# Optimization experiments

Measured on AMD Instinct MI355X. Metric: run time of the kernel, lower is better.

The kernel has to match this reference:

```python
import jax, jax.numpy as jnp
import numpy as np

B, LQ, LKV, D = 8, 2048, 2048, 1024

def setup_inputs() -> dict:
    key = jax.random.key(0)
    k1, k2, k3, k4, k5, k6, k7 = jax.random.split(key, 7)
    s = 1.0 / np.sqrt(D)
    return {
        "query": jax.random.normal(k1, (B, LQ, D), jnp.float32),
        "key": jax.random.normal(k2, (B, LKV, D), jnp.float32),
        "value": jax.random.normal(k3, (B, LKV, D), jnp.float32),
        "Wq": jax.random.uniform(k4, (D, D), jnp.float32, -s, s),
        "bq": jax.random.uniform(k5, (D,), jnp.float32, -s, s),
        "Wk": jax.random.uniform(k6, (D, D), jnp.float32, -s, s),
        "bk": jax.random.uniform(k7, (D,), jnp.float32, -s, s),
        "scale_factor": 32,
        "dropout_p": 0,
    }

def reference(query, key, value, Wq, bq, Wk, bk, scale_factor, dropout_p):
    # q/k linear projections (torch Linear: x @ W^T + b); v is used raw per the source
    q = jnp.einsum("bld,ed->ble", query, Wq) + bq
    k = jnp.einsum("bld,ed->ble", key, Wk) + bk
    scores = jnp.einsum("bqd,bkd->bqk", q, k) / jnp.float32(scale_factor)
    attn = jax.nn.softmax(scores, axis=-1)
    # dropout_p == 0 -> identity (deterministic baseline)
    return jnp.einsum("bqk,bkd->bqd", attn, value)
```

## Files before the change

### kernel.cpp

```cpp
#include <hip/hip_runtime.h>

typedef __bf16 bf16;
typedef __attribute__((ext_vector_type(4))) __bf16 bf16x4;
typedef __attribute__((ext_vector_type(8))) __bf16 bf16x8;
typedef __attribute__((ext_vector_type(4))) float f32x4;

__device__ __forceinline__ void gload_lds16(const void* g, void* l) {
  __builtin_amdgcn_global_load_lds(
      (const __attribute__((address_space(1))) unsigned int*)(unsigned long long)g,
      (__attribute__((address_space(3))) unsigned int*)(unsigned long long)l,
      16, 0, 0);
}

__global__ void cast_f32_bf16(const float* __restrict__ in, bf16* __restrict__ out, int n4) {
  int i = blockIdx.x * blockDim.x + threadIdx.x;
  if (i >= n4) return;
  float4 v = reinterpret_cast<const float4*>(in)[i];
  bf16x4 o;
  o[0] = (bf16)v.x; o[1] = (bf16)v.y; o[2] = (bf16)v.z; o[3] = (bf16)v.w;
  reinterpret_cast<bf16x4*>(out)[i] = o;
}

__global__ void transpose_cast(const float* __restrict__ V, bf16* __restrict__ VT,
                               int rows, int cols) {
  __shared__ bf16 tile[64][65];
  const int b = blockIdx.z;
  const float* Vb = V + (long)b * rows * cols;
  bf16* VTb = VT + (long)b * rows * cols;
  const int d0 = blockIdx.x * 64;
  const int k0 = blockIdx.y * 64;
  const int t = threadIdx.x;
  const int r = t >> 4;
  const int c4 = (t & 15) * 4;
#pragma unroll
  for (int p = 0; p < 4; ++p) {
    float4 v = *reinterpret_cast<const float4*>(&Vb[(long)(k0 + p * 16 + r) * cols + d0 + c4]);
    tile[p * 16 + r][c4 + 0] = (bf16)v.x;
    tile[p * 16 + r][c4 + 1] = (bf16)v.y;
    tile[p * 16 + r][c4 + 2] = (bf16)v.z;
    tile[p * 16 + r][c4 + 3] = (bf16)v.w;
  }
  __syncthreads();
#pragma unroll
  for (int p = 0; p < 4; ++p) {
    const int dd = p * 16 + r;
    bf16x4 o;
    o[0] = tile[c4 + 0][dd];
    o[1] = tile[c4 + 1][dd];
    o[2] = tile[c4 + 2][dd];
    o[3] = tile[c4 + 3][dd];
    *reinterpret_cast<bf16x4*>(&VTb[(long)(d0 + dd) * rows + k0 + c4]) = o;
  }
}

__global__ void softmax_rows(bf16* __restrict__ S) {
  const long row = blockIdx.x;
  bf16* p = S + row * 2048;
  const int t = threadIdx.x;
  const int wid = t >> 6;
  const int lane = t & 63;
  bf16x8 v = *reinterpret_cast<bf16x8*>(p + t * 8);
  float f[8];
  float m = -3.0e38f;
#pragma unroll
  for (int j = 0; j < 8; ++j) { f[j] = (float)v[j]; m = fmaxf(m, f[j]); }
#pragma unroll
  for (int off = 32; off >= 1; off >>= 1) m = fmaxf(m, __shfl_xor(m, off));
  __shared__ float redm[4], reds[4];
  if (lane == 0) redm[wid] = m;
  __syncthreads();
  m = fmaxf(fmaxf(redm[0], redm[1]), fmaxf(redm[2], redm[3]));
  float s = 0.f;
#pragma unroll
  for (int j = 0; j < 8; ++j) { f[j] = __expf(f[j] - m); s += f[j]; }
#pragma unroll
  for (int off = 32; off >= 1; off >>= 1) s += __shfl_xor(s, off);
  if (lane == 0) reds[wid] = s;
  __syncthreads();
  s = reds[0] + reds[1] + reds[2] + reds[3];
  const float inv = 1.0f / s;
  bf16x8 o;
#pragma unroll
  for (int j = 0; j < 8; ++j) o[j] = (bf16)(f[j] * inv);
  *reinterpret_cast<bf16x8*>(p + t * 8) = o;
}


#define BARRIER __builtin_amdgcn_s_barrier()
#define SCHED0 __builtin_amdgcn_sched_barrier(0)
#define VM4                                                \
  do {                                                     \
    asm volatile("s_waitcnt vmcnt(4)" ::: "memory");       \
  } while (0)

#define STAGE(buf, ko)                                     \
  {                                                        \
    bf16* l_ = ldsw + (buf) * 16384;                       \
    const long ko_ = (ko);                                 \
    gload_lds16(gA + ko_, l_);                             \
    gload_lds16(gA + ko_ + rK128, l_ + 4096);              \
    gload_lds16(gB + ko_, l_ + 8192);                      \
    gload_lds16(gB + ko_ + rK128, l_ + 12288);             \
  }

#define LOADA(dst, buf)                                                        \
  _Pragma("unroll") for (int m_ = 0; m_ < 8; ++m_)                             \
      dst[m_] = *reinterpret_cast<const bf16x8*>(aBase + (buf) * 16384 + m_ * 512);
#define LOADB(dst, buf)                                                        \
  _Pragma("unroll") for (int n_ = 0; n_ < 4; ++n_)                             \
      dst[n_] = *reinterpret_cast<const bf16x8*>(bBase + (buf) * 16384 + n_ * 512);

#define MFMA32(a_, b_)                                                         \
  _Pragma("unroll") for (int m_ = 0; m_ < 8; ++m_)                             \
  _Pragma("unroll") for (int n_ = 0; n_ < 4; ++n_)                             \
      acc[m_][n_] = __builtin_amdgcn_mfma_f32_16x16x32_bf16(                   \
          a_[m_], b_[n_], acc[m_][n_], 0, 0, 0);

#define ROT3 { int tmp_ = c0; c0 = c1; c1 = c2; c2 = tmp_; }

template <int MODE>
__global__ __launch_bounds__(512, 2)
void gemm_bt(const bf16* __restrict__ A, const bf16* __restrict__ Bm,
             const float* __restrict__ bias0, const float* __restrict__ bias1,
             void* __restrict__ Cvoid, const int* __restrict__ scale_ptr,
             int N, int K, long sA, long sB, long sC) {
  __shared__ bf16 lds[3][512][32];
  const int t = threadIdx.x;
  const int lane = t & 63;
  const int wid = t >> 6;
  const int wm = wid >> 2;
  const int wn = wid & 3;

  const int gx = gridDim.x, gy = gridDim.y;
  const int nwg = gx * gy * gridDim.z;
  int id = blockIdx.x + gx * (blockIdx.y + gy * blockIdx.z);
  {
    const int cpx = nwg >> 3;
    id = (id & 7) * cpx + (id >> 3);
  }
  const int bx = id % gx;
  const int by = (id / gx) % gy;
  const int bz = id / (gx * gy);

  const bf16* Ab = A + (long)bz * sA;
  const bf16* Bb = Bm + (long)bz * sB;
  const int tile_m = by * 256;
  const int tile_n = bx * 256;

  const int srow = t >> 2;
  const int soff = (((t & 3) ^ ((t >> 3) & 3)) << 3);
  const bf16* gA = Ab + (long)(tile_m + srow) * K + soff;
  const bf16* gB = Bb + (long)(tile_n + srow) * K + soff;
  const long rK128 = (long)K << 7;
  bf16* const ldsw = &lds[0][0][0] + wid * 512;

  const int frow = lane & 15;
  const int pko = (((lane >> 4) ^ ((lane >> 1) & 3)) << 3);
  const bf16* aBase = &lds[0][0][0] + (wm * 128 + frow) * 32 + pko;
  const bf16* bBase = &lds[0][0][0] + (256 + wn * 64 + frow) * 32 + pko;

  bf16x8 aX[8], bX[4], aY[8], bY[4];
  f32x4 acc[8][4] = {};

  const int NK = K >> 5;
  int c0 = 0, c1 = 1, c2 = 2;

  STAGE(0, 0)
  STAGE(1, 32)
  VM4;
  BARRIER;
  SCHED0;
  LOADA(aX, 0)
  LOADB(bX, 0)

  for (int kt = 0; kt < NK; kt += 2) {
    {
      const long tt = (kt + 2 < NK) ? (long)(kt + 2) : (long)(NK - 1);
      STAGE(c2, tt << 5)
    }
    VM4;
    BARRIER;
    SCHED0;
    LOADA(aY, c1)
    LOADB(bY, c1)
    MFMA32(aX, bX)
    ROT3
    {
      const long tt = (kt + 3 < NK) ? (long)(kt + 3) : (long)(NK - 1);
      STAGE(c2, tt << 5)
    }
    VM4;
    BARRIER;
    SCHED0;
    LOADA(aX, c1)
    LOADB(bX, c1)
    MFMA32(aY, bY)
    ROT3
  }

  float scl = 1.0f;
  if (MODE == 1) {
    const int iv = scale_ptr[0];
    const float fv = __int_as_float(iv);
    const float sv = (iv > 0 && iv < (1 << 20)) ? (float)iv : fv;
    scl = 1.0f / sv;
  }
  const int rb = tile_m + wm * 128 + ((lane >> 4) << 2);
  const int cb = tile_n + wn * 64 + (lane & 15);
  if (MODE == 2) {
    float* C = reinterpret_cast<float*>(Cvoid) + (long)bz * sC;
#pragma unroll
    for (int mf = 0; mf < 8; ++mf)
#pragma unroll
      for (int nf = 0; nf < 4; ++nf)
#pragma unroll
        for (int r = 0; r < 4; ++r)
          C[(long)(rb + mf * 16 + r) * N + (cb + nf * 16)] = acc[mf][nf][r];
  } else {
    bf16* C = reinterpret_cast<bf16*>(Cvoid) + (long)bz * sC;
    const float* bias = (MODE == 0) ? (bz ? bias1 : bias0) : nullptr;
#pragma unroll
    for (int nf = 0; nf < 4; ++nf) {
      const int col = cb + nf * 16;
      const float bv = (MODE == 0) ? bias[col] : 0.0f;
#pragma unroll
      for (int mf = 0; mf < 8; ++mf)
#pragma unroll
        for (int r = 0; r < 4; ++r)
          C[(long)(rb + mf * 16 + r) * N + col] = (bf16)(acc[mf][nf][r] * scl + bv);
    }
  }
}

extern "C" void kernel_launch(void* const* d_in, const int* in_sizes, int n_in,
                              void* d_out, int out_size, void* d_ws, size_t ws_size,
                              hipStream_t stream) {
  (void)in_sizes; (void)n_in; (void)out_size; (void)ws_size;
  const float* query = (const float*)d_in[0];
  const float* key   = (const float*)d_in[1];
  const float* value = (const float*)d_in[2];
  const float* Wq    = (const float*)d_in[3];
  const float* bq    = (const float*)d_in[4];
  const float* Wk    = (const float*)d_in[5];
  const float* bk    = (const float*)d_in[6];
  const int*   scale = (const int*)d_in[7];

  const int L = 2048, D = 1024;
  char* ws = (char*)d_ws;
  bf16* q_cast = (bf16*)ws;
  bf16* k_cast = q_cast + (long)16384 * 1024;
  bf16* S      = q_cast;
  bf16* Qp     = (bf16*)(ws + (size_t)67108864);
  bf16* Kp     = (bf16*)(ws + (size_t)100663296);
  bf16* VT     = (bf16*)(ws + (size_t)134217728);
  bf16* Wqb    = (bf16*)(ws + (size_t)167772160);
  bf16* Wkb    = (bf16*)(ws + (size_t)169869312);

  cast_f32_bf16<<<16384, 256, 0, stream>>>(query, q_cast, 4194304);
  cast_f32_bf16<<<16384, 256, 0, stream>>>(key,   k_cast, 4194304);
  cast_f32_bf16<<<1024,  256, 0, stream>>>(Wq, Wqb, 262144);
  cast_f32_bf16<<<1024,  256, 0, stream>>>(Wk, Wkb, 262144);
  transpose_cast<<<dim3(16, 32, 8), 256, 0, stream>>>(value, VT, 2048, 1024);

  gemm_bt<0><<<dim3(4, 64, 2), 512, 0, stream>>>(q_cast, Wqb, bq, bk, Qp, nullptr,
                                                 1024, 1024,
                                                 16777216L, 1048576L, 16777216L);
  gemm_bt<1><<<dim3(8, 8, 8), 512, 0, stream>>>(Qp, Kp, nullptr, nullptr, S, scale,
                                                2048, 1024,
                                                (long)L * D, (long)L * D, (long)L * L);
  softmax_rows<<<16384, 256, 0, stream>>>(S);
  gemm_bt<2><<<dim3(4, 8, 8), 512, 0, stream>>>(S, VT, nullptr, nullptr, d_out, nullptr,
                                                1024, 2048,
                                                (long)L * L, (long)D * L, (long)L * D);
}
```

Baseline: 299.9 us.

## Switch GEMM to 32x32x16 MFMA with 64-wide K double-buffered pipeline

Replaces the 16x16x32 MFMA tiles with 32x32x16 MFMA, so each wave holds 4x2 accumulators of 16 floats and reads fewer LDS fragments per FLOP. The K loop now stages 64-wide K chunks as two 32-wide halves into a double buffer, where the old code used a triple buffer of 32-wide chunks. It also adds explicit lgkmcnt waits and s_setprio around the MFMA blocks. The aim is to cut LDS read traffic and improve MFMA issue density, at the cost of extra barriers per iteration and a more serialized load-then-compute schedule.

```diff
diff --git a/kernel.cpp b/kernel.cpp
--- a/kernel.cpp
+++ b/kernel.cpp
@@ -3,7 +3,7 @@
 typedef __bf16 bf16;
 typedef __attribute__((ext_vector_type(4))) __bf16 bf16x4;
 typedef __attribute__((ext_vector_type(8))) __bf16 bf16x8;
-typedef __attribute__((ext_vector_type(4))) float f32x4;
+typedef __attribute__((ext_vector_type(16))) float f32x16;
 
 __device__ __forceinline__ void gload_lds16(const void* g, void* l) {
   __builtin_amdgcn_global_load_lds(
@@ -87,36 +87,53 @@
 
 
 #define BARRIER __builtin_amdgcn_s_barrier()
-#define SCHED0 __builtin_amdgcn_sched_barrier(0)
+#define LGKM0                                              \
+  do {                                                     \
+    asm volatile("s_waitcnt lgkmcnt(0)" ::: "memory");     \
+    __builtin_amdgcn_sched_barrier(0);                     \
+  } while (0)
 #define VM4                                                \
   do {                                                     \
     asm volatile("s_waitcnt vmcnt(4)" ::: "memory");       \
+    __builtin_amdgcn_sched_barrier(0);                     \
   } while (0)
-
-#define STAGE(buf, ko)                                     \
-  {                                                        \
-    bf16* l_ = ldsw + (buf) * 16384;                       \
-    const long ko_ = (ko);                                 \
-    gload_lds16(gA + ko_, l_);                             \
-    gload_lds16(gA + ko_ + rK128, l_ + 4096);              \
-    gload_lds16(gB + ko_, l_ + 8192);                      \
-    gload_lds16(gB + ko_ + rK128, l_ + 12288);             \
-  }
-
-#define LOADA(dst, buf)                                                        \
-  _Pragma("unroll") for (int m_ = 0; m_ < 8; ++m_)                             \
-      dst[m_] = *reinterpret_cast<const bf16x8*>(aBase + (buf) * 16384 + m_ * 512);
-#define LOADB(dst, buf)                                                        \
-  _Pragma("unroll") for (int n_ = 0; n_ < 4; ++n_)                             \
-      dst[n_] = *reinterpret_cast<const bf16x8*>(bBase + (buf) * 16384 + n_ * 512);
-
-#define MFMA32(a_, b_)                                                         \
-  _Pragma("unroll") for (int m_ = 0; m_ < 8; ++m_)                             \
-  _Pragma("unroll") for (int n_ = 0; n_ < 4; ++n_)                             \
-      acc[m_][n_] = __builtin_amdgcn_mfma_f32_16x16x32_bf16(                   \
-          a_[m_], b_[n_], acc[m_][n_], 0, 0, 0);
-
-#define ROT3 { int tmp_ = c0; c0 = c1; c1 = c2; c2 = tmp_; }
+#define VM0                                                \
+  do {                                                     \
+    asm volatile("s_waitcnt vmcnt(0)" ::: "memory");       \
+    __builtin_amdgcn_sched_barrier(0);                     \
+  } while (0)
+
+#define STAGEH(buf, kh, ko)                                     \
+  {                                                             \
+    bf16* lA_ = ldsw + ((buf) * 4 + (kh)) * 8192;               \
+    bf16* lB_ = ldsw + ((buf) * 4 + 2 + (kh)) * 8192;           \
+    const long g_ = (ko) + (kh) * 32;                           \
+    gload_lds16(gA + g_, lA_);                                  \
+    gload_lds16(gA + g_ + rK128, lA_ + 4096);                   \
+    gload_lds16(gB + g_, lB_);                                  \
+    gload_lds16(gB + g_ + rK128, lB_ + 4096);                   \
+  }
+
+#define LOADP(buf, kh)                                                         \
+  _Pragma("unroll") for (int m_ = 0; m_ < 4; ++m_) {                           \
+    const bf16* p_ = aB32 + ((buf) * 4 + (kh)) * 8192 + m_ * 1024;             \
+    a[m_][0] = *reinterpret_cast<const bf16x8*>(p_ + pk0);                     \
+    a[m_][1] = *reinterpret_cast<const bf16x8*>(p_ + pk1);                     \
+  }                                                                            \
+  _Pragma("unroll") for (int n_ = 0; n_ < 2; ++n_) {                           \
+    const bf16* p_ = bB32 + ((buf) * 4 + 2 + (kh)) * 8192 + n_ * 1024;         \
+    b[n_][0] = *reinterpret_cast<const bf16x8*>(p_ + pk0);                     \
+    b[n_][1] = *reinterpret_cast<const bf16x8*>(p_ + pk1);                     \
+  }
+
+#define MFMAP32                                                                \
+  _Pragma("unroll") for (int m_ = 0; m_ < 4; ++m_)                             \
+  _Pragma("unroll") for (int n_ = 0; n_ < 2; ++n_) {                           \
+    acc[m_][n_] = __builtin_amdgcn_mfma_f32_32x32x16_bf16(                     \
+        a[m_][0], b[n_][0], acc[m_][n_], 0, 0, 0);                             \
+    acc[m_][n_] = __builtin_amdgcn_mfma_f32_32x32x16_bf16(                     \
+        a[m_][1], b[n_][1], acc[m_][n_], 0, 0, 0);                             \
+  }
 
 template <int MODE>
 __global__ __launch_bounds__(512, 2)
@@ -124,7 +141,7 @@
              const float* __restrict__ bias0, const float* __restrict__ bias1,
              void* __restrict__ Cvoid, const int* __restrict__ scale_ptr,
              int N, int K, long sA, long sB, long sC) {
-  __shared__ bf16 lds[3][512][32];
+  __shared__ bf16 lds[8][256][32];
   const int t = threadIdx.x;
   const int lane = t & 63;
   const int wid = t >> 6;
@@ -154,49 +171,46 @@
   const long rK128 = (long)K << 7;
   bf16* const ldsw = &lds[0][0][0] + wid * 512;
 
-  const int frow = lane & 15;
-  const int pko = (((lane >> 4) ^ ((lane >> 1) & 3)) << 3);
-  const bf16* aBase = &lds[0][0][0] + (wm * 128 + frow) * 32 + pko;
-  const bf16* bBase = &lds[0][0][0] + (256 + wn * 64 + frow) * 32 + pko;
-
-  bf16x8 aX[8], bX[4], aY[8], bY[4];
-  f32x4 acc[8][4] = {};
-
-  const int NK = K >> 5;
-  int c0 = 0, c1 = 1, c2 = 2;
-
-  STAGE(0, 0)
-  STAGE(1, 32)
+  const int frow32 = lane & 31;
+  const int kcL = lane >> 5;
+  const int sw32 = (frow32 >> 1) & 3;
+  const int pk0 = ((kcL ^ sw32) << 3);
+  const int pk1 = (((2 + kcL) ^ sw32) << 3);
+  const bf16* aB32 = &lds[0][0][0] + (wm * 128 + frow32) * 32;
+  const bf16* bB32 = &lds[0][0][0] + (wn * 64 + frow32) * 32;
+
+  bf16x8 a[4][2], b[2][2];
+  f32x16 acc[4][2] = {};
+
+  STAGEH(0, 0, 0)
+  STAGEH(0, 1, 0)
   VM4;
   BARRIER;
-  SCHED0;
-  LOADA(aX, 0)
-  LOADB(bX, 0)
-
-  for (int kt = 0; kt < NK; kt += 2) {
-    {
-      const long tt = (kt + 2 < NK) ? (long)(kt + 2) : (long)(NK - 1);
-      STAGE(c2, tt << 5)
-    }
+
+  const int NK = K >> 6;
+  int c = 0;
+  for (int kt = 0; kt < NK; ++kt, c ^= 1) {
+    const long ko = (long)((kt + 1 < NK) ? (kt + 1) : kt) << 6;
+    LOADP(c, 0)
+    STAGEH(c ^ 1, 0, ko)
     VM4;
     BARRIER;
-    SCHED0;
-    LOADA(aY, c1)
-    LOADB(bY, c1)
-    MFMA32(aX, bX)
-    ROT3
-    {
-      const long tt = (kt + 3 < NK) ? (long)(kt + 3) : (long)(NK - 1);
-      STAGE(c2, tt << 5)
-    }
+    LGKM0;
+    __builtin_amdgcn_s_setprio(1);
+    MFMAP32
+    __builtin_amdgcn_s_setprio(0);
+    BARRIER;
+    LOADP(c, 1)
+    STAGEH(c ^ 1, 1, ko)
     VM4;
     BARRIER;
-    SCHED0;
-    LOADA(aX, c1)
-    LOADB(bX, c1)
-    MFMA32(aY, bY)
-    ROT3
-  }
+    LGKM0;
+    __builtin_amdgcn_s_setprio(1);
+    MFMAP32
+    __builtin_amdgcn_s_setprio(0);
+    BARRIER;
+  }
+  VM0;
 
   float scl = 1.0f;
   if (MODE == 1) {
@@ -205,29 +219,33 @@
     const float sv = (iv > 0 && iv < (1 << 20)) ? (float)iv : fv;
     scl = 1.0f / sv;
   }
-  const int rb = tile_m + wm * 128 + ((lane >> 4) << 2);
-  const int cb = tile_n + wn * 64 + (lane & 15);
+  const int rb = tile_m + wm * 128 + ((lane >> 5) << 2);
+  const int cb = tile_n + wn * 64 + (lane & 31);
   if (MODE == 2) {
     float* C = reinterpret_cast<float*>(Cvoid) + (long)bz * sC;
 #pragma unroll
-    for (int mf = 0; mf < 8; ++mf)
-#pragma unroll
-      for (int nf = 0; nf < 4; ++nf)
-#pragma unroll
-        for (int r = 0; r < 4; ++r)
-          C[(long)(rb + mf * 16 + r) * N + (cb + nf * 16)] = acc[mf][nf][r];
+    for (int mf = 0; mf < 4; ++mf)
+#pragma unroll
+      for (int nf = 0; nf < 2; ++nf)
+#pragma unroll
+        for (int rg = 0; rg < 16; ++rg) {
+          const int row = rb + mf * 32 + (rg & 3) + ((rg >> 2) << 3);
+          C[(long)row * N + cb + nf * 32] = acc[mf][nf][rg];
+        }
   } else {
     bf16* C = reinterpret_cast<bf16*>(Cvoid) + (long)bz * sC;
     const float* bias = (MODE == 0) ? (bz ? bias1 : bias0) : nullptr;
 #pragma unroll
-    for (int nf = 0; nf < 4; ++nf) {
-      const int col = cb + nf * 16;
+    for (int nf = 0; nf < 2; ++nf) {
+      const int col = cb + nf * 32;
       const float bv = (MODE == 0) ? bias[col] : 0.0f;
 #pragma unroll
-      for (int mf = 0; mf < 8; ++mf)
-#pragma unroll
-        for (int r = 0; r < 4; ++r)
-          C[(long)(rb + mf * 16 + r) * N + col] = (bf16)(acc[mf][nf][r] * scl + bv);
+      for (int mf = 0; mf < 4; ++mf)
+#pragma unroll
+        for (int rg = 0; rg < 16; ++rg) {
+          const int row = rb + mf * 32 + (rg & 3) + ((rg >> 2) << 3);
+          C[(long)row * N + col] = (bf16)(acc[mf][nf][rg] * scl + bv);
+        }
     }
   }
 }
```

After: 318.4 us. +6.1%, slower.
